# Performance work log

Hardware: AMD Instinct MI355X
Metric: run time of the kernel (lower is better)

Reference implementation:

```python
import jax, jax.numpy as jnp
import numpy as np

EPS = 1e-8


def _cdist(a, b):
    # a: [B,N,3], b: [B,M,3] -> euclidean distances [B,N,M]
    a2 = jnp.sum(a * a, axis=-1)[:, :, None]          # [B,N,1]
    b2 = jnp.sum(b * b, axis=-1)[:, None, :]          # [B,1,M]
    ab = jnp.einsum('bnd,bmd->bnm', a, b)             # [B,N,M]
    d2 = jnp.maximum(a2 + b2 - 2.0 * ab, 0.0)
    return jnp.sqrt(d2)


def setup_inputs() -> dict:
    key = jax.random.key(0)
    ks = jax.random.split(key, 8)
    B, N, M, C1, C2 = 16, 4096, 1024, 128, 256
    Cin = C1 + C2  # 384
    H1, H2 = 256, 128
    return {
        'xyz1': jax.random.normal(ks[0], (B, N, 3), dtype=jnp.float32),
        'xyz2': jax.random.normal(ks[1], (B, M, 3), dtype=jnp.float32),
        'points1': jax.random.normal(ks[2], (B, C1, N), dtype=jnp.float32),
        'points2': jax.random.normal(ks[3], (B, C2, M), dtype=jnp.float32),
        'W1': jax.random.normal(ks[4], (H1, Cin), dtype=jnp.float32) * (1.0 / np.sqrt(Cin)),
        'b1': jnp.zeros((H1,), dtype=jnp.float32),
        'W2': jax.random.normal(ks[5], (H2, H1), dtype=jnp.float32) * (1.0 / np.sqrt(H1)),
        'b2': jnp.zeros((H2,), dtype=jnp.float32),
    }


def reference(xyz1, xyz2, points1, points2, W1, b1, W2, b2):
    # inverse-distance weighted interpolation over ALL M source points
    dist = _cdist(xyz1, xyz2) + EPS                   # [B,N,M]
    inv = 1.0 / dist
    weight = inv / jnp.sum(inv, axis=-1, keepdims=True)
    # interpolated features: [B,N,M] @ [B,M,C2] -> [B,C2,N]
    interpolated = jnp.einsum('bnm,bcm->bcn', weight, points2)
    new_points = jnp.concatenate([points1, interpolated], axis=1)  # [B,C1+C2,N]
    # 1x1 Conv1d MLP with ReLU
    h = jax.nn.relu(jnp.einsum('oc,bcn->bon', W1, new_points) + b1[None, :, None])
    out = jax.nn.relu(jnp.einsum('oc,bcn->bon', W2, h) + b2[None, :, None])
    return out
```

## Files before the change

### kernel.cpp

```cpp
#include <hip/hip_runtime.h>
#include <math.h>

#define BBATCH 16
#define NPTS   4096
#define MPTS   1024
#define C1c    128
#define C2c    256
#define CINc   384
#define H1c    256
#define H2c    128
#define TN     64

typedef _Float16 f16x8 __attribute__((ext_vector_type(8)));
typedef _Float16 f16x4 __attribute__((ext_vector_type(4)));
typedef float    f32x4 __attribute__((ext_vector_type(4)));

#define INV_HALF   8192
#define OFF_XYZ2   32768
#define OFF_RED    49152
#define SMEM_BYTES 51200

#define NFRAG_P2  (BBATCH * 32 * 16 * 64)
#define NFRAG_W1  (16 * 12 * 64)
#define NFRAG_W2  (8 * 8 * 64)
#define WS_P2S  0
#define WS_W1S  (NFRAG_P2 * 8)
#define WS_W2S  (WS_W1S + NFRAG_W1 * 8)
#define WS_F16_TOTAL (WS_W2S + NFRAG_W2 * 8)

__global__ __launch_bounds__(256) void cvt_swz(
    const float* __restrict__ p2, const float* __restrict__ W1,
    const float* __restrict__ W2, _Float16* __restrict__ ws)
{
    const int t = blockIdx.x * 256 + threadIdx.x;
    const float* src;
    _Float16* dst;
    if (t < NFRAG_P2) {
        const int lane = t & 63, wt = (t >> 6) & 15, s = (t >> 10) & 31, b = t >> 15;
        const int c = wt * 16 + (lane & 15);
        const int m = s * 32 + (lane >> 4) * 8;
        src = p2 + ((size_t)(b * C2c + c)) * MPTS + m;
        dst = ws + WS_P2S + (size_t)t * 8;
    } else if (t < NFRAG_P2 + NFRAG_W1) {
        const int u = t - NFRAG_P2;
        const int lane = u & 63, kc = (u >> 6) % 12, wt = (u >> 6) / 12;
        const int o = wt * 16 + (lane & 15);
        const int k = kc * 32 + (lane >> 4) * 8;
        src = W1 + (size_t)o * CINc + k;
        dst = ws + WS_W1S + (size_t)u * 8;
    } else {
        const int v = t - NFRAG_P2 - NFRAG_W1;
        const int lane = v & 63, oc = (v >> 6) & 7, wt2 = v >> 9;
        const int o = wt2 * 16 + (lane & 15);
        const int k = oc * 32 + (lane >> 4) * 8;
        src = W2 + (size_t)o * H1c + k;
        dst = ws + WS_W2S + (size_t)v * 8;
    }
    const float4 a0 = *(const float4*)(src);
    const float4 a1 = *(const float4*)(src + 4);
    f16x8 h;
    h[0] = (_Float16)a0.x; h[1] = (_Float16)a0.y; h[2] = (_Float16)a0.z; h[3] = (_Float16)a0.w;
    h[4] = (_Float16)a1.x; h[5] = (_Float16)a1.y; h[6] = (_Float16)a1.z; h[7] = (_Float16)a1.w;
    *(f16x8*)dst = h;
}

template <bool F16P>
__global__ __launch_bounds__(512, 4) void fp_mfma11(
    const float* __restrict__ xyz1, const float* __restrict__ xyz2,
    const float* __restrict__ p1,   const float* __restrict__ p2,
    const float* __restrict__ W1,   const float* __restrict__ b1v,
    const float* __restrict__ W2,   const float* __restrict__ b2v,
    const _Float16* __restrict__ p2s, const _Float16* __restrict__ W1s,
    const _Float16* __restrict__ W2s,
    float* __restrict__ out)
{
    __shared__ __align__(16) char smem[SMEM_BYTES];
    _Float16* s_inv  = (_Float16*)smem;
    _Float16* s_X    = (_Float16*)smem;
    _Float16* s_H    = (_Float16*)smem;
    float*    s_xyz2 = (float*)(smem + OFF_XYZ2);
    float*    s_red  = (float*)(smem + OFF_RED);

    const int tid  = threadIdx.x;
    const int w    = tid >> 6;
    const int L    = tid & 63;
    const int quad = L >> 4;
    const int l16  = L & 15;

    const int id = blockIdx.x;
    const int b  = (id & 7) * 2 + ((id >> 3) & 1);
    const int n0 = (id >> 4) * TN;

    const float* __restrict__ z2b = xyz2 + (size_t)b * MPTS * 3;
    const float* __restrict__ p2b = p2   + (size_t)b * C2c * MPTS;
    const _Float16* __restrict__ p2sb =
        F16P ? (p2s + (((size_t)b * 32 * 16 + (size_t)w * 2) * 64 + L) * 8) : (const _Float16*)nullptr;

    for (int i = tid; i < MPTS * 3 / 4; i += 512)
        ((f32x4*)s_xyz2)[i] = ((const f32x4*)z2b)[i];

    const float x1x = xyz1[((size_t)b * NPTS + n0 + L) * 3 + 0];
    const float x1y = xyz1[((size_t)b * NPTS + n0 + L) * 3 + 1];
    const float x1z = xyz1[((size_t)b * NPTS + n0 + L) * 3 + 2];

    f32x4 acc[2][4];
    #pragma unroll
    for (int ct = 0; ct < 2; ++ct)
        #pragma unroll
        for (int nt = 0; nt < 4; ++nt)
            acc[ct][nt] = (f32x4){0.f, 0.f, 0.f, 0.f};

    float ssum = 0.f;
    f16x8 Aa[2][2];

    auto loadA = [&](int s, f16x8 dst[2]) {
        if (F16P) {
            const _Float16* ap = p2sb + (size_t)s * (16 * 64 * 8);
            #pragma unroll
            for (int ct = 0; ct < 2; ++ct)
                dst[ct] = *(const f16x8*)(ap + (size_t)ct * (64 * 8));
        } else {
            const float* ap = p2b + (size_t)(w * 32 + l16) * MPTS + s * 32 + quad * 8;
            #pragma unroll
            for (int ct = 0; ct < 2; ++ct) {
                const float4 a0 = *(const float4*)(ap + (size_t)ct * (16 * MPTS));
                const float4 a1 = *(const float4*)(ap + (size_t)ct * (16 * MPTS) + 4);
                f16x8 h;
                h[0] = (_Float16)a0.x; h[1] = (_Float16)a0.y; h[2] = (_Float16)a0.z; h[3] = (_Float16)a0.w;
                h[4] = (_Float16)a1.x; h[5] = (_Float16)a1.y; h[6] = (_Float16)a1.z; h[7] = (_Float16)a1.w;
                dst[ct] = h;
            }
        }
    };

    auto gen_g = [&](int ss_, int g) {
        _Float16* buf = s_inv + (ss_ & 1) * INV_HALF;
        const float* zp = s_xyz2 + (size_t)(ss_ * 128 + w * 16 + g * 8) * 3;
        f32x4 zr[6];
        #pragma unroll
        for (int j = 0; j < 6; ++j) zr[j] = ((const f32x4*)zp)[j];
        const float* zv = (const float*)zr;
        f16x8 iv;
        #pragma unroll
        for (int i = 0; i < 8; ++i) {
            const float dx = x1x - zv[3 * i + 0];
            const float dy = x1y - zv[3 * i + 1];
            const float dz = x1z - zv[3 * i + 2];
            const float d2 = fmaf(dx, dx, fmaf(dy, dy, fmaf(dz, dz, 1e-12f)));
            const float inv = __builtin_amdgcn_rsqf(d2);
            ssum += inv;
            iv[i] = (_Float16)inv;
        }
        *(f16x8*)(buf + ((((w >> 1) * 4 + quad) * 64) + ((w & 1) * 2 + g) * 16 + l16) * 8) = iv;
    };

    loadA(0, Aa[0]);
    __syncthreads();
    gen_g(0, 0);
    gen_g(0, 1);
    __syncthreads();

    for (int ss = 0; ss < 8; ++ss) {
        const _Float16* buf = s_inv + (ss & 1) * INV_HALF;
        #pragma unroll
        for (int cc = 0; cc < 4; ++cc) {
            const int s = ss * 4 + cc;
            if (s + 1 < 32) loadA(s + 1, Aa[(cc + 1) & 1]);
            if (ss + 1 < 8 && cc < 2) gen_g(ss + 1, cc);
            __builtin_amdgcn_s_setprio(1);
            #pragma unroll
            for (int nt = 0; nt < 4; ++nt) {
                const f16x8 bf = *(const f16x8*)(buf + ((cc * 4 + nt) * 64 + L) * 8);
                #pragma unroll
                for (int ct = 0; ct < 2; ++ct)
                    acc[ct][nt] = __builtin_amdgcn_mfma_f32_16x16x32_f16(Aa[cc & 1][ct], bf, acc[ct][nt], 0, 0, 0);
            }
            __builtin_amdgcn_s_setprio(0);
        }
        __syncthreads();
    }

    {
        #pragma unroll
        for (int h = 0; h < 2; ++h) {
            const int f  = w * 2 + h;
            const int kq = f >> 2, nt = f & 3;
            const float* pp = p1 + ((size_t)b * C1c + kq * 32 + quad * 8) * NPTS + n0 + nt * 16 + l16;
            float tv[8];
            #pragma unroll
            for (int j = 0; j < 8; ++j) tv[j] = pp[(size_t)j * NPTS];
            f16x8 v;
            #pragma unroll
            for (int j = 0; j < 8; ++j) v[j] = (_Float16)tv[j];
            *(f16x8*)(s_X + ((size_t)f * 64 + L) * 8) = v;
        }
    }

    s_red[tid] = ssum;
    __syncthreads();
    if (tid < 64) {
        float s = 0.f;
        #pragma unroll
        for (int wv = 0; wv < 8; ++wv) s += s_red[wv * 64 + tid];
        s_red[tid] = 1.0f / s;
    }
    __syncthreads();

    {
        float rn4[4];
        #pragma unroll
        for (int nt = 0; nt < 4; ++nt) rn4[nt] = s_red[nt * 16 + l16];
        #pragma unroll
        for (int ct = 0; ct < 2; ++ct) {
            const int kq = 4 + w;
            const int lp = (ct * 2 + (quad >> 1)) * 16 + l16;
            const int jo = (quad & 1) * 4;
            #pragma unroll
            for (int nt = 0; nt < 4; ++nt) {
                const f32x4 v = acc[ct][nt];
                const float r = rn4[nt];
                f16x4 hv;
                hv[0] = (_Float16)(v[0] * r);
                hv[1] = (_Float16)(v[1] * r);
                hv[2] = (_Float16)(v[2] * r);
                hv[3] = (_Float16)(v[3] * r);
                *(f16x4*)(s_X + (((size_t)(kq * 4 + nt)) * 64 + lp) * 8 + jo) = hv;
            }
        }
    }
    __syncthreads();

    f32x4 hacc[2][4];
    #pragma unroll
    for (int ct = 0; ct < 2; ++ct)
        #pragma unroll
        for (int nt = 0; nt < 4; ++nt)
            hacc[ct][nt] = (f32x4){0.f, 0.f, 0.f, 0.f};

    auto loadW1 = [&](int kc, f16x8 dst[2]) {
        if (F16P) {
            const _Float16* wp = W1s + (((size_t)(w * 2) * 12 + kc) * 64 + L) * 8;
            #pragma unroll
            for (int ct = 0; ct < 2; ++ct)
                dst[ct] = *(const f16x8*)(wp + (size_t)ct * (12 * 64 * 8));
        } else {
            const float* wp = W1 + (size_t)(w * 32 + l16) * CINc + kc * 32 + quad * 8;
            #pragma unroll
            for (int ct = 0; ct < 2; ++ct) {
                const float4 a0 = *(const float4*)(wp + ct * (16 * CINc));
                const float4 a1 = *(const float4*)(wp + ct * (16 * CINc) + 4);
                f16x8 h;
                h[0] = (_Float16)a0.x; h[1] = (_Float16)a0.y; h[2] = (_Float16)a0.z; h[3] = (_Float16)a0.w;
                h[4] = (_Float16)a1.x; h[5] = (_Float16)a1.y; h[6] = (_Float16)a1.z; h[7] = (_Float16)a1.w;
                dst[ct] = h;
            }
        }
    };

    {
        f16x8 afP[2][2];
        loadW1(0, afP[0]);
        #pragma unroll
        for (int kc = 0; kc < 12; ++kc) {
            if (kc + 1 < 12) loadW1(kc + 1, afP[(kc + 1) & 1]);
            __builtin_amdgcn_s_setprio(1);
            #pragma unroll
            for (int nt = 0; nt < 4; ++nt) {
                const f16x8 bf = *(const f16x8*)(s_X + (((size_t)(kc * 4 + nt)) * 64 + L) * 8);
                #pragma unroll
                for (int ct = 0; ct < 2; ++ct)
                    hacc[ct][nt] = __builtin_amdgcn_mfma_f32_16x16x32_f16(afP[kc & 1][ct], bf, hacc[ct][nt], 0, 0, 0);
            }
            __builtin_amdgcn_s_setprio(0);
        }
    }

    __syncthreads();

    {
        f32x4 bb[2];
        #pragma unroll
        for (int ct = 0; ct < 2; ++ct)
            bb[ct] = *(const f32x4*)(b1v + w * 32 + ct * 16 + quad * 4);
        #pragma unroll
        for (int ct = 0; ct < 2; ++ct) {
            const int lp = (ct * 2 + (quad >> 1)) * 16 + l16;
            const int jo = (quad & 1) * 4;
            #pragma unroll
            for (int nt = 0; nt < 4; ++nt) {
                const f32x4 v = hacc[ct][nt];
                f16x4 hv;
                hv[0] = (_Float16)fmaxf(v[0] + bb[ct][0], 0.f);
                hv[1] = (_Float16)fmaxf(v[1] + bb[ct][1], 0.f);
                hv[2] = (_Float16)fmaxf(v[2] + bb[ct][2], 0.f);
                hv[3] = (_Float16)fmaxf(v[3] + bb[ct][3], 0.f);
                *(f16x4*)(s_H + (((size_t)(w * 4 + nt)) * 64 + lp) * 8 + jo) = hv;
            }
        }
    }
    __syncthreads();

    f32x4 oacc[4];
    #pragma unroll
    for (int nt = 0; nt < 4; ++nt)
        oacc[nt] = (f32x4){0.f, 0.f, 0.f, 0.f};

    auto loadW2 = [&](int oc, f16x8& dst) {
        if (F16P) {
            dst = *(const f16x8*)(W2s + (((size_t)(w * 8 + oc)) * 64 + L) * 8);
        } else {
            const float* wp = W2 + (size_t)(w * 16 + l16) * H1c + oc * 32 + quad * 8;
            const float4 a0 = *(const float4*)(wp);
            const float4 a1 = *(const float4*)(wp + 4);
            f16x8 h;
            h[0] = (_Float16)a0.x; h[1] = (_Float16)a0.y; h[2] = (_Float16)a0.z; h[3] = (_Float16)a0.w;
            h[4] = (_Float16)a1.x; h[5] = (_Float16)a1.y; h[6] = (_Float16)a1.z; h[7] = (_Float16)a1.w;
            dst = h;
        }
    };

    {
        f16x8 afP2[2];
        loadW2(0, afP2[0]);
        #pragma unroll
        for (int oc = 0; oc < 8; ++oc) {
            if (oc + 1 < 8) loadW2(oc + 1, afP2[(oc + 1) & 1]);
            __builtin_amdgcn_s_setprio(1);
            #pragma unroll
            for (int nt = 0; nt < 4; ++nt) {
                const f16x8 bf = *(const f16x8*)(s_H + (((size_t)(oc * 4 + nt)) * 64 + L) * 8);
                oacc[nt] = __builtin_amdgcn_mfma_f32_16x16x32_f16(afP2[oc & 1], bf, oacc[nt], 0, 0, 0);
            }
            __builtin_amdgcn_s_setprio(0);
        }
    }

    {
        const f32x4 bb2 = *(const f32x4*)(b2v + w * 16 + quad * 4);
        #pragma unroll
        for (int nt = 0; nt < 4; ++nt) {
            float* op = out + ((size_t)b * H2c + w * 16 + quad * 4) * NPTS
                            + n0 + nt * 16 + l16;
            #pragma unroll
            for (int j = 0; j < 4; ++j)
                op[(size_t)j * NPTS] = fmaxf(oacc[nt][j] + bb2[j], 0.f);
        }
    }
}

extern "C" void kernel_launch(void* const* d_in, const int* in_sizes, int n_in,
                              void* d_out, int out_size, void* d_ws, size_t ws_size,
                              hipStream_t stream) {
    (void)in_sizes; (void)n_in; (void)out_size;
    const float* xyz1 = (const float*)d_in[0];
    const float* xyz2 = (const float*)d_in[1];
    const float* p1   = (const float*)d_in[2];
    const float* p2   = (const float*)d_in[3];
    const float* W1   = (const float*)d_in[4];
    const float* b1   = (const float*)d_in[5];
    const float* W2   = (const float*)d_in[6];
    const float* b2   = (const float*)d_in[7];
    float* out = (float*)d_out;

    dim3 grid(BBATCH * (NPTS / TN));
    dim3 block(512);
    if (ws_size >= (size_t)WS_F16_TOTAL * 2) {
        _Float16* ws = (_Float16*)d_ws;
        const int nswz = NFRAG_P2 + NFRAG_W1 + NFRAG_W2;
        cvt_swz<<<dim3(nswz / 256), dim3(256), 0, stream>>>(p2, W1, W2, ws);
        fp_mfma11<true><<<grid, block, 0, stream>>>(xyz1, xyz2, p1, p2, W1, b1, W2, b2,
                                                    ws + WS_P2S, ws + WS_W1S, ws + WS_W2S, out);
    } else {
        fp_mfma11<false><<<grid, block, 0, stream>>>(xyz1, xyz2, p1, p2, W1, b1, W2, b2,
                                                     nullptr, nullptr, nullptr, out);
    }
}
```

Baseline: 162.6 us.

## Deepen A-fragment prefetch, peel last stage, hoist p1/W1/W2 loads, lighter barriers

Prefetches the points2 MFMA fragments two steps ahead using a 4-slot register ring instead of double-buffering. The final interpolation stage is peeled so the points1 global loads are issued before its MFMAs and overlap with them. The first W1 and W2 fragment loads are hoisted ahead of the preceding LDS epilogues. __syncthreads is replaced with a barrier that waits only on lgkmcnt, so it no longer waits for outstanding global loads. The added live registers risk occupancy at 512 threads with a minimum of 4 blocks.

After: 161.9 us. No clear change (-0.4%).

```diff
diff --git a/kernel.cpp b/kernel.cpp
--- a/kernel.cpp
+++ b/kernel.cpp
@@ -14,6 +14,9 @@
 typedef _Float16 f16x8 __attribute__((ext_vector_type(8)));
 typedef _Float16 f16x4 __attribute__((ext_vector_type(4)));
 typedef float    f32x4 __attribute__((ext_vector_type(4)));
+
+#define BAR() do { asm volatile("s_waitcnt lgkmcnt(0)" ::: "memory"); \
+                   __builtin_amdgcn_s_barrier(); } while (0)
 
 #define INV_HALF   8192
 #define OFF_XYZ2   32768
@@ -65,7 +68,7 @@
 }
 
 template <bool F16P>
-__global__ __launch_bounds__(512, 4) void fp_mfma11(
+__global__ __launch_bounds__(512, 4) void fp_mfma12(
     const float* __restrict__ xyz1, const float* __restrict__ xyz2,
     const float* __restrict__ p1,   const float* __restrict__ p2,
     const float* __restrict__ W1,   const float* __restrict__ b1v,
@@ -111,7 +114,7 @@
             acc[ct][nt] = (f32x4){0.f, 0.f, 0.f, 0.f};
 
     float ssum = 0.f;
-    f16x8 Aa[2][2];
+    f16x8 Aa[4][2];
 
     auto loadA = [&](int s, f16x8 dst[2]) {
         if (F16P) {
@@ -155,56 +158,101 @@
     };
 
     loadA(0, Aa[0]);
-    __syncthreads();
+    loadA(1, Aa[1]);
+    BAR();
     gen_g(0, 0);
     gen_g(0, 1);
-    __syncthreads();
-
-    for (int ss = 0; ss < 8; ++ss) {
+    BAR();
+
+    for (int ss = 0; ss < 7; ++ss) {
         const _Float16* buf = s_inv + (ss & 1) * INV_HALF;
         #pragma unroll
         for (int cc = 0; cc < 4; ++cc) {
             const int s = ss * 4 + cc;
-            if (s + 1 < 32) loadA(s + 1, Aa[(cc + 1) & 1]);
-            if (ss + 1 < 8 && cc < 2) gen_g(ss + 1, cc);
+            loadA(s + 2, Aa[(cc + 2) & 3]);
+            if (cc < 2) gen_g(ss + 1, cc);
             __builtin_amdgcn_s_setprio(1);
             #pragma unroll
             for (int nt = 0; nt < 4; ++nt) {
                 const f16x8 bf = *(const f16x8*)(buf + ((cc * 4 + nt) * 64 + L) * 8);
                 #pragma unroll
                 for (int ct = 0; ct < 2; ++ct)
-                    acc[ct][nt] = __builtin_amdgcn_mfma_f32_16x16x32_f16(Aa[cc & 1][ct], bf, acc[ct][nt], 0, 0, 0);
+                    acc[ct][nt] = __builtin_amdgcn_mfma_f32_16x16x32_f16(Aa[cc][ct], bf, acc[ct][nt], 0, 0, 0);
             }
             __builtin_amdgcn_s_setprio(0);
         }
-        __syncthreads();
-    }
-
+        BAR();
+    }
+
+    float tv[2][8];
     {
         #pragma unroll
         for (int h = 0; h < 2; ++h) {
             const int f  = w * 2 + h;
             const int kq = f >> 2, nt = f & 3;
             const float* pp = p1 + ((size_t)b * C1c + kq * 32 + quad * 8) * NPTS + n0 + nt * 16 + l16;
-            float tv[8];
-            #pragma unroll
-            for (int j = 0; j < 8; ++j) tv[j] = pp[(size_t)j * NPTS];
+            #pragma unroll
+            for (int j = 0; j < 8; ++j) tv[h][j] = pp[(size_t)j * NPTS];
+        }
+    }
+    {
+        const _Float16* buf = s_inv + INV_HALF;
+        #pragma unroll
+        for (int cc = 0; cc < 4; ++cc) {
+            if (cc < 2) loadA(28 + cc + 2, Aa[(cc + 2) & 3]);
+            __builtin_amdgcn_s_setprio(1);
+            #pragma unroll
+            for (int nt = 0; nt < 4; ++nt) {
+                const f16x8 bf = *(const f16x8*)(buf + ((cc * 4 + nt) * 64 + L) * 8);
+                #pragma unroll
+                for (int ct = 0; ct < 2; ++ct)
+                    acc[ct][nt] = __builtin_amdgcn_mfma_f32_16x16x32_f16(Aa[cc][ct], bf, acc[ct][nt], 0, 0, 0);
+            }
+            __builtin_amdgcn_s_setprio(0);
+        }
+    }
+    {
+        #pragma unroll
+        for (int h = 0; h < 2; ++h) {
+            const int f = w * 2 + h;
             f16x8 v;
             #pragma unroll
-            for (int j = 0; j < 8; ++j) v[j] = (_Float16)tv[j];
+            for (int j = 0; j < 8; ++j) v[j] = (_Float16)tv[h][j];
             *(f16x8*)(s_X + ((size_t)f * 64 + L) * 8) = v;
         }
     }
-
     s_red[tid] = ssum;
-    __syncthreads();
+    BAR();
+
     if (tid < 64) {
         float s = 0.f;
         #pragma unroll
         for (int wv = 0; wv < 8; ++wv) s += s_red[wv * 64 + tid];
         s_red[tid] = 1.0f / s;
     }
-    __syncthreads();
+    BAR();
+
+    f16x8 afP[2][2];
+    auto loadW1 = [&](int kc, f16x8 dst[2]) {
+        if (F16P) {
+            const _Float16* wp = W1s + (((size_t)(w * 2) * 12 + kc) * 64 + L) * 8;
+            #pragma unroll
+            for (int ct = 0; ct < 2; ++ct)
+                dst[ct] = *(const f16x8*)(wp + (size_t)ct * (12 * 64 * 8));
+        } else {
+            const float* wp = W1 + (size_t)(w * 32 + l16) * CINc + kc * 32 + quad * 8;
+            #pragma unroll
+            for (int ct = 0; ct < 2; ++ct) {
+                const float4 a0 = *(const float4*)(wp + ct * (16 * CINc));
+                const float4 a1 = *(const float4*)(wp + ct * (16 * CINc) + 4);
+                f16x8 h;
+                h[0] = (_Float16)a0.x; h[1] = (_Float16)a0.y; h[2] = (_Float16)a0.z; h[3] = (_Float16)a0.w;
+                h[4] = (_Float16)a1.x; h[5] = (_Float16)a1.y; h[6] = (_Float16)a1.z; h[7] = (_Float16)a1.w;
+                dst[ct] = h;
+            }
+        }
+    };
+    loadW1(0, afP[0]);
 
     {
         float rn4[4];
@@ -228,7 +276,7 @@
             }
         }
     }
-    __syncthreads();
+    BAR();
 
     f32x4 hacc[2][4];
     #pragma unroll
@@ -237,74 +285,23 @@
         for (int nt = 0; nt < 4; ++nt)
             hacc[ct][nt] = (f32x4){0.f, 0.f, 0.f, 0.f};
 
-    auto loadW1 = [&](int kc, f16x8 dst[2]) {
-        if (F16P) {
-            const _Float16* wp = W1s + (((size_t)(w * 2) * 12 + kc) * 64 + L) * 8;
+    #pragma unroll
+    for (int kc = 0; kc < 12; ++kc) {
+        if (kc + 1 < 12) loadW1(kc + 1, afP[(kc + 1) & 1]);
+        __builtin_amdgcn_s_setprio(1);
+        #pragma unroll
+        for (int nt = 0; nt < 4; ++nt) {
+            const f16x8 bf = *(const f16x8*)(s_X + (((size_t)(kc * 4 + nt)) * 64 + L) * 8);
             #pragma unroll
             for (int ct = 0; ct < 2; ++ct)
-                dst[ct] = *(const f16x8*)(wp + (size_t)ct * (12 * 64 * 8));
-        } else {
-            const float* wp = W1 + (size_t)(w * 32 + l16) * CINc + kc * 32 + quad * 8;
-            #pragma unroll
-            for (int ct = 0; ct < 2; ++ct) {
-                const float4 a0 = *(const float4*)(wp + ct * (16 * CINc));
-                const float4 a1 = *(const float4*)(wp + ct * (16 * CINc) + 4);
-                f16x8 h;
-                h[0] = (_Float16)a0.x; h[1] = (_Float16)a0.y; h[2] = (_Float16)a0.z; h[3] = (_Float16)a0.w;
-                h[4] = (_Float16)a1.x; h[5] = (_Float16)a1.y; h[6] = (_Float16)a1.z; h[7] = (_Float16)a1.w;
-                dst[ct] = h;
-            }
-        }
-    };
-
-    {
-        f16x8 afP[2][2];
-        loadW1(0, afP[0]);
-        #pragma unroll
-        for (int kc = 0; kc < 12; ++kc) {
-            if (kc + 1 < 12) loadW1(kc + 1, afP[(kc + 1) & 1]);
-            __builtin_amdgcn_s_setprio(1);
-            #pragma unroll
-            for (int nt = 0; nt < 4; ++nt) {
-                const f16x8 bf = *(const f16x8*)(s_X + (((size_t)(kc * 4 + nt)) * 64 + L) * 8);
-                #pragma unroll
-                for (int ct = 0; ct < 2; ++ct)
-                    hacc[ct][nt] = __builtin_amdgcn_mfma_f32_16x16x32_f16(afP[kc & 1][ct], bf, hacc[ct][nt], 0, 0, 0);
-            }
-            __builtin_amdgcn_s_setprio(0);
-        }
-    }
-
-    __syncthreads();
-
-    {
-        f32x4 bb[2];
-        #pragma unroll
-        for (int ct = 0; ct < 2; ++ct)
-            bb[ct] = *(const f32x4*)(b1v + w * 32 + ct * 16 + quad * 4);
-        #pragma unroll
-        for (int ct = 0; ct < 2; ++ct) {
-            const int lp = (ct * 2 + (quad >> 1)) * 16 + l16;
-            const int jo = (quad & 1) * 4;
-            #pragma unroll
-            for (int nt = 0; nt < 4; ++nt) {
-                const f32x4 v = hacc[ct][nt];
-                f16x4 hv;
-                hv[0] = (_Float16)fmaxf(v[0] + bb[ct][0], 0.f);
-                hv[1] = (_Float16)fmaxf(v[1] + bb[ct][1], 0.f);
-                hv[2] = (_Float16)fmaxf(v[2] + bb[ct][2], 0.f);
-                hv[3] = (_Float16)fmaxf(v[3] + bb[ct][3], 0.f);
-                *(f16x4*)(s_H + (((size_t)(w * 4 + nt)) * 64 + lp) * 8 + jo) = hv;
-            }
-        }
-    }
-    __syncthreads();
-
-    f32x4 oacc[4];
-    #pragma unroll
-    for (int nt = 0; nt < 4; ++nt)
-        oacc[nt] = (f32x4){0.f, 0.f, 0.f, 0.f};
-
+                hacc[ct][nt] = __builtin_amdgcn_mfma_f32_16x16x32_f16(afP[kc & 1][ct], bf, hacc[ct][nt], 0, 0, 0);
+        }
+        __builtin_amdgcn_s_setprio(0);
+    }
+
+    BAR();
+
+    f16x8 afP2[2];
     auto loadW2 = [&](int oc, f16x8& dst) {
         if (F16P) {
             dst = *(const f16x8*)(W2s + (((size_t)(w * 8 + oc)) * 64 + L) * 8);
@@ -318,21 +315,46 @@
             dst = h;
         }
     };
-
-    {
-        f16x8 afP2[2];
-        loadW2(0, afP2[0]);
-        #pragma unroll
-        for (int oc = 0; oc < 8; ++oc) {
-            if (oc + 1 < 8) loadW2(oc + 1, afP2[(oc + 1) & 1]);
-            __builtin_amdgcn_s_setprio(1);
+    loadW2(0, afP2[0]);
+
+    {
+        f32x4 bb[2];
+        #pragma unroll
+        for (int ct = 0; ct < 2; ++ct)
+            bb[ct] = *(const f32x4*)(b1v + w * 32 + ct * 16 + quad * 4);
+        #pragma unroll
+        for (int ct = 0; ct < 2; ++ct) {
+            const int lp = (ct * 2 + (quad >> 1)) * 16 + l16;
+            const int jo = (quad & 1) * 4;
             #pragma unroll
             for (int nt = 0; nt < 4; ++nt) {
-                const f16x8 bf = *(const f16x8*)(s_H + (((size_t)(oc * 4 + nt)) * 64 + L) * 8);
-                oacc[nt] = __builtin_amdgcn_mfma_f32_16x16x32_f16(afP2[oc & 1], bf, oacc[nt], 0, 0, 0);
-            }
-            __builtin_amdgcn_s_setprio(0);
-        }
+                const f32x4 v = hacc[ct][nt];
+                f16x4 hv;
+                hv[0] = (_Float16)fmaxf(v[0] + bb[ct][0], 0.f);
+                hv[1] = (_Float16)fmaxf(v[1] + bb[ct][1], 0.f);
+                hv[2] = (_Float16)fmaxf(v[2] + bb[ct][2], 0.f);
+                hv[3] = (_Float16)fmaxf(v[3] + bb[ct][3], 0.f);
+                *(f16x4*)(s_H + (((size_t)(w * 4 + nt)) * 64 + lp) * 8 + jo) = hv;
+            }
+        }
+    }
+    BAR();
+
+    f32x4 oacc[4];
+    #pragma unroll
+    for (int nt = 0; nt < 4; ++nt)
+        oacc[nt] = (f32x4){0.f, 0.f, 0.f, 0.f};
+
+    #pragma unroll
+    for (int oc = 0; oc < 8; ++oc) {
+        if (oc + 1 < 8) loadW2(oc + 1, afP2[(oc + 1) & 1]);
+        __builtin_amdgcn_s_setprio(1);
+        #pragma unroll
+        for (int nt = 0; nt < 4; ++nt) {
+            const f16x8 bf = *(const f16x8*)(s_H + (((size_t)(oc * 4 + nt)) * 64 + L) * 8);
+            oacc[nt] = __builtin_amdgcn_mfma_f32_16x16x32_f16(afP2[oc & 1], bf, oacc[nt], 0, 0, 0);
+        }
+        __builtin_amdgcn_s_setprio(0);
     }
 
     {
@@ -368,10 +390,10 @@
         _Float16* ws = (_Float16*)d_ws;
         const int nswz = NFRAG_P2 + NFRAG_W1 + NFRAG_W2;
         cvt_swz<<<dim3(nswz / 256), dim3(256), 0, stream>>>(p2, W1, W2, ws);
-        fp_mfma11<true><<<grid, block, 0, stream>>>(xyz1, xyz2, p1, p2, W1, b1, W2, b2,
+        fp_mfma12<true><<<grid, block, 0, stream>>>(xyz1, xyz2, p1, p2, W1, b1, W2, b2,
                                                     ws + WS_P2S, ws + WS_W1S, ws + WS_W2S, out);
     } else {
-        fp_mfma11<false><<<grid, block, 0, stream>>>(xyz1, xyz2, p1, p2, W1, b1, W2, b2,
+        fp_mfma12<false><<<grid, block, 0, stream>>>(xyz1, xyz2, p1, p2, W1, b1, W2, b2,
                                                      nullptr, nullptr, nullptr, out);
     }
 }
```
